# Kernel optimization log

Hardware: AMD Instinct MI355X
Metric: run time of the kernel (lower is better)

The kernel has to match this reference:

```python
import jax, jax.numpy as jnp
import numpy as np

B, S, H, NH, NL = 8, 768, 768, 12, 5
HD = H // NH


def setup_inputs() -> dict:
    key = jax.random.key(0)
    ks = jax.random.split(key, 14)
    lim = 1.0 / np.sqrt(H)
    u = lambda k, shape: jax.random.uniform(k, shape, jnp.float32, -lim, lim)
    inp = {}
    inp["hidden_states"] = jax.random.normal(ks[0], (B, S, H), jnp.float32)
    inp["language_ids"] = jax.random.randint(ks[1], (B,), 0, NL)
    inp["attention_mask"] = jnp.ones((B, S), jnp.int32)
    # per-language query/key Linear weights (torch Linear: y = x @ W.T + b)
    inp["Wq_lang"] = u(ks[2], (NL, H, H))
    inp["bq_lang"] = u(ks[3], (NL, H))
    inp["Wk_lang"] = u(ks[4], (NL, H, H))
    inp["bk_lang"] = u(ks[5], (NL, H))
    # nn.MultiheadAttention params
    inp["in_proj_w"] = u(ks[6], (3 * H, H))
    inp["in_proj_b"] = u(ks[7], (3 * H,))
    inp["out_proj_w"] = u(ks[8], (H, H))
    inp["out_proj_b"] = u(ks[9], (H,))
    # alignment matrices: initialized as eye in torch; perturb so products are non-trivial
    inp["align"] = jnp.eye(H, dtype=jnp.float32) + 0.02 * jax.random.normal(ks[10], (NL, NL, H, H), jnp.float32)
    # output projection + layer norm
    inp["proj_w"] = u(ks[11], (H, H))
    inp["proj_b"] = u(ks[12], (H,))
    inp["ln_g"] = jnp.ones((H,), jnp.float32)
    inp["ln_b"] = jnp.zeros((H,), jnp.float32)
    return inp


def reference(hidden_states, language_ids, attention_mask, Wq_lang, bq_lang, Wk_lang, bk_lang,
              in_proj_w, in_proj_b, out_proj_w, out_proj_b, align, proj_w, proj_b, ln_g, ln_b):
    b, s, h = hidden_states.shape
    lang = language_ids
    # language-routed query/key transforms (grouped GEMM via gather of per-lang weights)
    q = jnp.einsum('bsi,boi->bso', hidden_states, Wq_lang[lang]) + bq_lang[lang][:, None, :]
    k = jnp.einsum('bsi,boi->bso', hidden_states, Wk_lang[lang]) + bk_lang[lang][:, None, :]
    # nn.MultiheadAttention (eval mode, no dropout). Note: the torch module's
    # key_padding_mask is always all-False due to a masked_fill(-inf).bool() bug,
    # so no masking is applied -- reproduced faithfully here.
    wq, wk, wv = jnp.split(in_proj_w, 3, axis=0)
    bq_, bk_, bv_ = jnp.split(in_proj_b, 3)
    Q = (jnp.einsum('bsi,oi->bso', q, wq) + bq_).reshape(b, s, NH, HD)
    K = (jnp.einsum('bsi,oi->bso', k, wk) + bk_).reshape(b, s, NH, HD)
    V = (jnp.einsum('bsi,oi->bso', hidden_states, wv) + bv_).reshape(b, s, NH, HD)
    scores = jnp.einsum('bqhd,bkhd->bhqk', Q, K) / np.sqrt(HD).astype(np.float32)
    attn = jax.nn.softmax(scores, axis=-1)  # [b, nh, s, s]
    ctx = jnp.einsum('bhqk,bkhd->bqhd', attn, V).reshape(b, s, h)
    aligned = jnp.einsum('bsi,oi->bso', ctx, out_proj_w) + out_proj_b
    # pairwise alignment chain: for each i, aligned_i @ prod_{j: lang_j != lang_i} A[lang_i, lang_j]
    # (i==j skipped; same-language pairs skipped since no A exists)
    same = lang[:, None] == lang[None, :]  # [b, b]; diagonal is True -> identity
    sel = align[lang[:, None], lang[None, :]]  # [b, b, h, h]
    I = jnp.eye(h, dtype=hidden_states.dtype)
    Smat = jnp.where(same[:, :, None, None], I, sel)  # [b(i), b(j), h, h]
    def step(carry, Sj):  # carry [b,h,h], Sj [b,h,h] for one j across all i
        return carry @ Sj, None
    M, _ = jax.lax.scan(step, jnp.tile(I, (b, 1, 1)), jnp.swapaxes(Smat, 0, 1))
    aligned = jnp.einsum('bsh,bhk->bsk', aligned, M)
    # output projection + residual layer norm
    out = jnp.einsum('bsi,oi->bso', aligned, proj_w) + proj_b
    x = out + hidden_states
    mu = x.mean(-1, keepdims=True)
    var = x.var(-1, keepdims=True)
    return (x - mu) / jnp.sqrt(var + 1e-5) * ln_g + ln_b
```

## Files before the change

### kernel.cpp

```cpp
#include <hip/hip_runtime.h>

#define Bn 8
#define Sn 768
#define Hn 768
#define NHn 12
#define HDn 64
#define NLn 5

typedef unsigned short u16;
typedef __bf16 bf16x8 __attribute__((ext_vector_type(8)));
typedef short s16x8 __attribute__((ext_vector_type(8)));
typedef float f32x4 __attribute__((ext_vector_type(4)));
typedef unsigned short u16x4 __attribute__((ext_vector_type(4)));

static __device__ __forceinline__ float bf2f(u16 v) {
    return __uint_as_float(((unsigned)v) << 16);
}
static __device__ __forceinline__ u16 f2bf(float f) {
    unsigned u = __float_as_uint(f);
    unsigned r = u + 0x7fffu + ((u >> 16) & 1u);
    return (u16)(r >> 16);
}
static __device__ __forceinline__ bf16x8 ld8(const u16* p) {
    return *reinterpret_cast<const bf16x8*>(p);
}
static __device__ __forceinline__ void glds16(const u16* g, u16* l) {
    __builtin_amdgcn_global_load_lds(
        (const __attribute__((address_space(1))) void*)g,
        (__attribute__((address_space(3))) void*)l, 16, 0, 0);
}

#define PREP_NF2B 6912
#define PREP_NTR  1584
__global__ __launch_bounds__(256) void k_prep(
    const float* __restrict__ hidden, u16* __restrict__ hb,
    const float* __restrict__ ipw, u16* __restrict__ ipwb,
    const float* __restrict__ projw, u16* __restrict__ pjwb,
    const float* __restrict__ Wq, const float* __restrict__ Wk,
    const float* __restrict__ opw, u16* __restrict__ S, u16* __restrict__ opwT,
    const float* __restrict__ ipb,
    const float* __restrict__ bq_lang, const float* __restrict__ bk_lang,
    float* __restrict__ beff)
{
    __shared__ float T[64][65];
    const size_t HH = (size_t)Hn * Hn;
    const int bid = blockIdx.x, tid = threadIdx.x;
    if (bid < PREP_NF2B) {
        const int n0 = (int)(Bn * Sn * Hn / 4), n1 = (int)(3 * HH / 4), n2 = (int)(HH / 4);
        int i = bid * 256 + tid;
        const float* s; u16* d; int off;
        if (i < n0)                { s = hidden; d = hb;   off = i; }
        else if (i < n0 + n1)      { s = ipw;    d = ipwb; off = i - n0; }
        else if (i < n0 + n1 + n2) { s = projw;  d = pjwb; off = i - n0 - n1; }
        else return;
        float4 v = reinterpret_cast<const float4*>(s)[off];
        u16x4 o;
        o[0] = f2bf(v.x); o[1] = f2bf(v.y); o[2] = f2bf(v.z); o[3] = f2bf(v.w);
        reinterpret_cast<u16x4*>(d)[off] = o;
    } else if (bid < PREP_NF2B + PREP_NTR) {
        int b2 = bid - PREP_NF2B;
        int z = b2 / 144, r = b2 % 144;
        int bx = r % 12, by = r / 12;
        const float* src;
        u16* dst;
        if (z < 5)       { src = Wq + (size_t)z * HH;       dst = S + (size_t)z * HH; }
        else if (z < 10) { src = Wk + (size_t)(z - 5) * HH; dst = S + (size_t)z * HH; }
        else             { src = opw;                        dst = opwT; }
        int i0 = bx * 64, o0 = by * 64;
        int x = tid & 63, ys = tid >> 6;
        for (int rr = ys; rr < 64; rr += 4)
            T[rr][x] = src[(size_t)(o0 + rr) * Hn + i0 + x];
        __syncthreads();
        for (int rr = ys; rr < 64; rr += 4)
            dst[(size_t)(i0 + rr) * Hn + o0 + x] = f2bf(T[x][rr]);
    } else {
        int b3 = bid - PREP_NF2B - PREP_NTR;
        int ox = b3 % 3, y = b3 / 3;
        int o = ox * 256 + tid;
        int which = y / 5, l = y % 5;
        const float4* w = reinterpret_cast<const float4*>(ipw + (size_t)which * HH + (size_t)o * Hn);
        const float4* bv = reinterpret_cast<const float4*>(((which ? bk_lang : bq_lang) + (size_t)l * Hn));
        float s = 0.f;
        for (int j = 0; j < Hn / 4; ++j) {
            float4 a = w[j], b = bv[j];
            s += a.x * b.x + a.y * b.y + a.z * b.z + a.w * b.w;
        }
        s += ipb[which * Hn + o];
        beff[(size_t)(which * 5 + l) * Hn + o] = s;
    }
}

template<int TM>
__device__ __forceinline__ void gemm_core(
    const u16* __restrict__ A, int lda,
    const u16* __restrict__ Bw, int ldb,
    const float* __restrict__ bias,
    const float* __restrict__ addres,
    u16* __restrict__ outH, float* __restrict__ outF,
    u16* __restrict__ outVT, int ldc,
    int m0, int n0, float scale)
{
    constexpr int MI = TM / 32;
    constexpr int AIT = TM / 64;
    __shared__ u16 As[3 * TM * 32];
    __shared__ u16 Bs[3 * 128 * 32];
    const int tid = threadIdx.x;
    const int lane = tid & 63, wave = tid >> 6;
    const int lrow = lane & 15, lquad = lane >> 4;
    const int wm = (wave >> 1) * (TM / 2), wn = (wave & 1) * 64;

    const u16* gA = A + (size_t)(m0 + (tid >> 2)) * lda + (tid & 3) * 8;
    const u16* gB = Bw + (size_t)(n0 + (tid >> 2)) * ldb + (tid & 3) * 8;

    f32x4 z = {0.f, 0.f, 0.f, 0.f};
    f32x4 acc[MI][4];
    #pragma unroll
    for (int i = 0; i < MI; ++i)
        #pragma unroll
        for (int j = 0; j < 4; ++j) acc[i][j] = z;

    auto stage = [&](int bs, int k0) {
        #pragma unroll
        for (int it = 0; it < AIT; ++it)
            glds16(gA + (size_t)(it * 64) * lda + k0, &As[bs * TM * 32 + (tid + 256 * it) * 8]);
        #pragma unroll
        for (int it = 0; it < 2; ++it)
            glds16(gB + (size_t)(it * 64) * ldb + k0, &Bs[bs * 128 * 32 + (tid + 256 * it) * 8]);
    };
    auto compute = [&](int bc) {
        const u16* Ab = &As[bc * TM * 32];
        const u16* Bb = &Bs[bc * 128 * 32];
        bf16x8 af[MI], bf_[4];
        #pragma unroll
        for (int i = 0; i < MI; ++i)
            af[i] = ld8(&Ab[(wm + i * 16 + lrow) * 32 + lquad * 8]);
        #pragma unroll
        for (int j = 0; j < 4; ++j)
            bf_[j] = ld8(&Bb[(wn + j * 16 + lrow) * 32 + lquad * 8]);
        #pragma unroll
        for (int i = 0; i < MI; ++i)
            #pragma unroll
            for (int j = 0; j < 4; ++j)
                acc[i][j] = __builtin_amdgcn_mfma_f32_16x16x32_bf16(af[i], bf_[j], acc[i][j], 0, 0, 0);
    };

    stage(0, 0);
    stage(1, 32);
    int bc = 0, bs = 2;
    for (int kt = 0; kt < 24; ++kt) {
        if (kt < 23) {
            if constexpr (TM == 256) {
                asm volatile("s_waitcnt vmcnt(6)" ::: "memory");
            } else {
                asm volatile("s_waitcnt vmcnt(4)" ::: "memory");
            }
        } else {
            asm volatile("s_waitcnt vmcnt(0)" ::: "memory");
        }
        __builtin_amdgcn_s_barrier();
        if (kt < 22) {
            stage(bs, (kt + 2) * 32);
            bs = (bs == 2) ? 0 : bs + 1;
        }
        compute(bc);
        bc = (bc == 2) ? 0 : bc + 1;
    }

    #pragma unroll
    for (int i = 0; i < MI; ++i) {
        #pragma unroll
        for (int j = 0; j < 4; ++j) {
            int col = n0 + wn + j * 16 + lrow;
            float bv = bias ? bias[col] : 0.f;
            if (outVT) {
                int row0 = m0 + wm + i * 16 + lquad * 4;
                int bb = row0 / Sn, s = row0 % Sn;
                int hh = col >> 6, dd = col & 63;
                u16x4 o;
                #pragma unroll
                for (int r = 0; r < 4; ++r) o[r] = f2bf((acc[i][j][r] + bv) * scale);
                *reinterpret_cast<u16x4*>(
                    outVT + (((size_t)bb * NHn + hh) * 64 + dd) * Sn + s) = o;
            } else {
                #pragma unroll
                for (int r = 0; r < 4; ++r) {
                    int row = m0 + wm + i * 16 + lquad * 4 + r;
                    float v = (acc[i][j][r] + bv) * scale;
                    if (addres) v += addres[(size_t)row * ldc + col];
                    if (outF) outF[(size_t)row * ldc + col] = v;
                    else      outH[(size_t)row * ldc + col] = f2bf(v);
                }
            }
        }
    }
}

__device__ __forceinline__ void gemm64(
    const u16* __restrict__ A, const u16* __restrict__ Bw,
    u16* __restrict__ outH, int m0, int n0)
{
    __shared__ u16 As[3 * 64 * 32];
    __shared__ u16 Bs[3 * 64 * 32];
    const int tid = threadIdx.x;
    const int lane = tid & 63, wave = tid >> 6;
    const int lrow = lane & 15, lquad = lane >> 4;
    const int wm = (wave >> 1) * 32, wn = (wave & 1) * 32;

    const u16* gA = A + (size_t)(m0 + (tid >> 2)) * Hn + (tid & 3) * 8;
    const u16* gB = Bw + (size_t)(n0 + (tid >> 2)) * Hn + (tid & 3) * 8;

    f32x4 z = {0.f, 0.f, 0.f, 0.f};
    f32x4 acc[2][2];
    #pragma unroll
    for (int i = 0; i < 2; ++i)
        #pragma unroll
        for (int j = 0; j < 2; ++j) acc[i][j] = z;

    auto stage = [&](int bs, int k0) {
        glds16(gA + k0, &As[bs * 64 * 32 + tid * 8]);
        glds16(gB + k0, &Bs[bs * 64 * 32 + tid * 8]);
    };
    auto compute = [&](int bc) {
        const u16* Ab = &As[bc * 64 * 32];
        const u16* Bb = &Bs[bc * 64 * 32];
        bf16x8 af[2], bf_[2];
        #pragma unroll
        for (int i = 0; i < 2; ++i)
            af[i] = ld8(&Ab[(wm + i * 16 + lrow) * 32 + lquad * 8]);
        #pragma unroll
        for (int j = 0; j < 2; ++j)
            bf_[j] = ld8(&Bb[(wn + j * 16 + lrow) * 32 + lquad * 8]);
        #pragma unroll
        for (int i = 0; i < 2; ++i)
            #pragma unroll
            for (int j = 0; j < 2; ++j)
                acc[i][j] = __builtin_amdgcn_mfma_f32_16x16x32_bf16(af[i], bf_[j], acc[i][j], 0, 0, 0);
    };

    stage(0, 0);
    stage(1, 32);
    int bc = 0, bs = 2;
    for (int kt = 0; kt < 24; ++kt) {
        if (kt < 23) {
            asm volatile("s_waitcnt vmcnt(2)" ::: "memory");
        } else {
            asm volatile("s_waitcnt vmcnt(0)" ::: "memory");
        }
        __builtin_amdgcn_s_barrier();
        if (kt < 22) {
            stage(bs, (kt + 2) * 32);
            bs = (bs == 2) ? 0 : bs + 1;
        }
        compute(bc);
        bc = (bc == 2) ? 0 : bc + 1;
    }

    #pragma unroll
    for (int i = 0; i < 2; ++i)
        #pragma unroll
        for (int j = 0; j < 2; ++j) {
            int col = n0 + wn + j * 16 + lrow;
            #pragma unroll
            for (int r = 0; r < 4; ++r) {
                int row_ = m0 + wm + i * 16 + lquad * 4 + r;
                outH[(size_t)row_ * Hn + col] = f2bf(acc[i][j][r]);
            }
        }
}


__global__ __launch_bounds__(256, 2) void k_gemm_qkv(
    const u16* __restrict__ A,
    const u16* __restrict__ Sq, const u16* __restrict__ Sk,
    const u16* __restrict__ Wv,
    const float* __restrict__ beff, const float* __restrict__ ipb,
    const int* __restrict__ lang,
    u16* __restrict__ outQ, u16* __restrict__ outK, u16* __restrict__ outVT)
{
    const size_t HH = (size_t)Hn * Hn;
    int z = blockIdx.z;
    int m0 = blockIdx.x * 256, n0 = blockIdx.y * 128;
    int l = lang[blockIdx.x / 3];
    if (z == 0) {
        gemm_core<256>(A, Hn, Sq + (size_t)l * HH, Hn, beff + (size_t)l * Hn,
                       nullptr, outQ, nullptr, nullptr, Hn, m0, n0, 0.125f);
    } else if (z == 1) {
        gemm_core<256>(A, Hn, Sk + (size_t)l * HH, Hn, beff + (size_t)(5 + l) * Hn,
                       nullptr, outK, nullptr, nullptr, Hn, m0, n0, 1.f);
    } else {
        gemm_core<256>(A, Hn, Wv, Hn, ipb + 2 * Hn,
                       nullptr, nullptr, nullptr, outVT, Hn, m0, n0, 1.f);
    }
}

__global__ __launch_bounds__(256) void k_comb10(
    const u16* __restrict__ ipwb, u16* __restrict__ S)
{
    const size_t HH = (size_t)Hn * Hn;
    int z = blockIdx.z;
    const u16* Aop = ipwb + (z < 5 ? 0 : HH);
    gemm_core<128>(Aop, Hn, S + (size_t)z * HH, Hn, nullptr, nullptr,
                   S + (size_t)(10 + z) * HH, nullptr, nullptr, Hn,
                   blockIdx.x * 128, blockIdx.y * 128, 1.f);
}

__global__ __launch_bounds__(256) void k_chain_first(
    const u16* __restrict__ alignb, const int* __restrict__ lang,
    u16* __restrict__ out5)
{
    const size_t HH = (size_t)Hn * Hn;
    int l = blockIdx.z, lj = lang[Bn - 1];
    u16* dst = out5 + (size_t)l * HH;
    int i0 = blockIdx.x * 64, o0 = blockIdx.y * 64;
    const int tid = threadIdx.x;
    if (lj == l) {
        #pragma unroll
        for (int it = 0; it < 2; ++it) {
            int s = tid + 256 * it;
            int ri = s >> 3, c8 = s & 7;
            s16x8 v;
            #pragma unroll
            for (int e = 0; e < 8; ++e)
                v[e] = (short)((i0 + ri == o0 + c8 * 8 + e) ? 0x3F80 : 0);
            *reinterpret_cast<s16x8*>(dst + (size_t)(i0 + ri) * Hn + o0 + c8 * 8) = v;
        }
    } else {
        const u16* src = alignb + ((size_t)l * NLn + lj) * HH;
        __shared__ u16 T[64][72];
        #pragma unroll
        for (int it = 0; it < 2; ++it) {
            int s = tid + 256 * it;
            int r = s >> 3, c8 = s & 7;
            s16x8 v = *reinterpret_cast<const s16x8*>(
                src + (size_t)(o0 + r) * Hn + i0 + c8 * 8);
            #pragma unroll
            for (int e = 0; e < 8; ++e) T[c8 * 8 + e][r] = (u16)v[e];
        }
        __syncthreads();
        #pragma unroll
        for (int it = 0; it < 2; ++it) {
            int s = tid + 256 * it;
            int ri = s >> 3, c8 = s & 7;
            s16x8 v = *reinterpret_cast<const s16x8*>(&T[ri][c8 * 8]);
            *reinterpret_cast<s16x8*>(dst + (size_t)(i0 + ri) * Hn + o0 + c8 * 8) = v;
        }
    }
}

__global__ __launch_bounds__(256) void k_chain64(
    const u16* __restrict__ Pin, u16* __restrict__ Pout,
    const u16* __restrict__ alignb, const int* __restrict__ lang, int j)
{
    const size_t HH = (size_t)Hn * Hn;
    int l = blockIdx.z;
    int lj = lang[j];
    const u16* Pl = Pin + (size_t)l * HH;
    u16* Po = Pout + (size_t)l * HH;
    int m0 = blockIdx.x * 64, n0 = blockIdx.y * 64;
    if (lj == l) {
        int tid = threadIdx.x;
        #pragma unroll
        for (int it = 0; it < 2; ++it) {
            int s = tid + 256 * it;
            int row = s >> 3, seg = s & 7;
            *reinterpret_cast<s16x8*>(Po + (size_t)(m0 + row) * Hn + n0 + seg * 8) =
                *reinterpret_cast<const s16x8*>(Pl + (size_t)(m0 + row) * Hn + n0 + seg * 8);
        }
    } else {
        const u16* F = alignb + ((size_t)l * NLn + lj) * HH;
        gemm64(Pl, F, Po, m0, n0);
    }
}

__global__ __launch_bounds__(256) void k_uop(
    const u16* __restrict__ opwT, const u16* __restrict__ MT5,
    const float* __restrict__ opb,
    u16* __restrict__ U5, float* __restrict__ opbeff)
{
    const size_t HH = (size_t)Hn * Hn;
    int bid = blockIdx.x;
    if (bid < 720) {
        int z = bid / 144, r = bid % 144;
        gemm64(opwT, MT5 + (size_t)z * HH, U5 + (size_t)z * HH,
               (r % 12) * 64, (r / 12) * 64);
    } else {
        int b2 = bid - 720;
        int n = (b2 % 3) * 256 + threadIdx.x;
        int l = b2 / 3;
        const u16* mt = MT5 + ((size_t)l * Hn + n) * Hn;
        float s = 0.f;
        for (int k = 0; k < Hn; k += 8) {
            s16x8 v = *reinterpret_cast<const s16x8*>(mt + k);
            #pragma unroll
            for (int j = 0; j < 8; ++j) s += opb[k + j] * bf2f((u16)v[j]);
        }
        opbeff[(size_t)l * Hn + n] = s;
    }
}

__global__ __launch_bounds__(256) void k_wb2(
    const u16* __restrict__ pjwb, const u16* __restrict__ U5,
    const float* __restrict__ opbeff, const float* __restrict__ projw,
    const float* __restrict__ projb,
    u16* __restrict__ W5, float* __restrict__ bias2)
{
    const size_t HH = (size_t)Hn * Hn;
    int bid = blockIdx.x;
    if (bid < 720) {
        int z = bid / 144, r = bid % 144;
        gemm64(pjwb, U5 + (size_t)z * HH, W5 + (size_t)z * HH,
               (r % 12) * 64, (r / 12) * 64);
    } else {
        int b2 = bid - 720;
        int m = (b2 % 3) * 256 + threadIdx.x;
        int l = b2 / 3;
        const float4* w = reinterpret_cast<const float4*>(projw + (size_t)m * Hn);
        const float4* ob = reinterpret_cast<const float4*>(opbeff + (size_t)l * Hn);
        float s = 0.f;
        for (int j = 0; j < Hn / 4; ++j) {
            float4 a = w[j], b = ob[j];
            s += a.x * b.x + a.y * b.y + a.z * b.z + a.w * b.w;
        }
        bias2[(size_t)l * Hn + m] = s + projb[m];
    }
}

__global__ __launch_bounds__(256) void k_xfused(
    const u16* __restrict__ ctx, const u16* __restrict__ W5,
    const float* __restrict__ bias2, const int* __restrict__ lang,
    const float* __restrict__ hidden, float* __restrict__ x)
{
    int l = lang[blockIdx.x / 6];
    gemm_core<128>(ctx, Hn, W5 + (size_t)l * Hn * Hn, Hn, bias2 + (size_t)l * Hn,
                   hidden, nullptr, x, nullptr, Hn,
                   blockIdx.x * 128, blockIdx.y * 128, 1.f);
}

__global__ __launch_bounds__(512) void k_attn_conv(
    const u16* __restrict__ Q, const u16* __restrict__ K,
    const u16* __restrict__ VT, u16* __restrict__ ctx,
    const float* __restrict__ alignf, u16* __restrict__ alignb)
{
    __shared__ u16 Ks[2][64 * 64];
    __shared__ u16 Vs[2][64 * 64];
    __shared__ u16 Pw[8][16 * 72];

    const int bid = blockIdx.x, tid = threadIdx.x;
    if (bid >= 576) {
        int base = (bid - 576) * 4096 + tid;
        #pragma unroll
        for (int it = 0; it < 8; ++it) {
            int i = base + it * 512;
            float4 v = reinterpret_cast<const float4*>(alignf)[i];
            u16x4 o;
            o[0] = f2bf(v.x); o[1] = f2bf(v.y); o[2] = f2bf(v.z); o[3] = f2bf(v.w);
            reinterpret_cast<u16x4*>(alignb)[i] = o;
        }
        return;
    }

    const int q0 = (bid % 6) * 128, h = (bid / 6) % NHn, bz = bid / 72;
    const int wave = tid >> 6, lane = tid & 63;
    const int lrow = lane & 15, lquad = lane >> 4;
    const int sw = lrow & 7;

    const u16* Qp = Q + ((size_t)(bz * Sn + q0 + wave * 16 + lrow)) * Hn + h * HDn;
    const u16* Kb = K + (size_t)bz * Sn * Hn + h * HDn;
    const u16* Vb = VT + ((size_t)(bz * NHn + h) * 64) * Sn;

    bf16x8 qa0 = ld8(Qp + lquad * 8);
    bf16x8 qa1 = ld8(Qp + 32 + lquad * 8);

    f32x4 z4 = {0.f, 0.f, 0.f, 0.f};
    float m_r[4], l_l[4];
    f32x4 oacc[4];
    #pragma unroll
    for (int r = 0; r < 4; ++r) { m_r[r] = -1e30f; l_l[r] = 0.f; }
    #pragma unroll
    for (int jd = 0; jd < 4; ++jd) oacc[jd] = z4;

    const int krow = tid >> 3, kp = (tid & 7) ^ (krow & 7);
    const u16* kg = Kb + (size_t)krow * Hn + kp * 8;
    const u16* vg = Vb + (size_t)krow * Sn + kp * 8;

    auto stage = [&](int bs, int t0) {
        glds16(kg + (size_t)t0 * Hn, &Ks[bs][tid * 8]);
        glds16(vg + t0, &Vs[bs][tid * 8]);
    };

    auto compute = [&](int bc) {
        f32x4 sc[4];
        __builtin_amdgcn_s_setprio(1);
        #pragma unroll
        for (int j = 0; j < 4; ++j) {
            int base = (j * 16 + lrow) * 64 + ((lquad ^ sw) * 8);
            f32x4 s = __builtin_amdgcn_mfma_f32_16x16x32_bf16(qa0, ld8(&Ks[bc][base]), z4, 0, 0, 0);
            sc[j] = __builtin_amdgcn_mfma_f32_16x16x32_bf16(qa1, ld8(&Ks[bc][base ^ 32]), s, 0, 0, 0);
        }
        __builtin_amdgcn_s_setprio(0);
        float tmax[4];
        #pragma unroll
        for (int r = 0; r < 4; ++r)
            tmax[r] = fmaxf(fmaxf(sc[0][r], sc[1][r]), fmaxf(sc[2][r], sc[3][r]));
        #pragma unroll
        for (int off = 1; off < 16; off <<= 1)
            #pragma unroll
            for (int r = 0; r < 4; ++r)
                tmax[r] = fmaxf(tmax[r], __shfl_xor(tmax[r], off));
        bool grow = (tmax[0] > m_r[0] + 8.f) | (tmax[1] > m_r[1] + 8.f) |
                    (tmax[2] > m_r[2] + 8.f) | (tmax[3] > m_r[3] + 8.f);
        if (grow) {
            #pragma unroll
            for (int r = 0; r < 4; ++r) {
                float mn = fmaxf(m_r[r], tmax[r]);
                float a = __expf(m_r[r] - mn);
                m_r[r] = mn;
                l_l[r] *= a;
                #pragma unroll
                for (int jd = 0; jd < 4; ++jd) oacc[jd][r] *= a;
            }
        }
        float ps[4] = {0.f, 0.f, 0.f, 0.f};
        #pragma unroll
        for (int j = 0; j < 4; ++j)
            #pragma unroll
            for (int r = 0; r < 4; ++r) {
                float p = __expf(sc[j][r] - m_r[r]);
                ps[r] += p;
                Pw[wave][(lquad * 4 + r) * 72 + j * 16 + lrow] = f2bf(p);
            }
        #pragma unroll
        for (int r = 0; r < 4; ++r) l_l[r] += ps[r];
        bf16x8 pa0 = ld8(&Pw[wave][lrow * 72 + lquad * 8]);
        bf16x8 pa1 = ld8(&Pw[wave][lrow * 72 + 32 + lquad * 8]);
        __builtin_amdgcn_s_setprio(1);
        #pragma unroll
        for (int jd = 0; jd < 4; ++jd) {
            int vbase = (jd * 16 + lrow) * 64 + ((lquad ^ sw) * 8);
            oacc[jd] = __builtin_amdgcn_mfma_f32_16x16x32_bf16(pa0, ld8(&Vs[bc][vbase]), oacc[jd], 0, 0, 0);
            oacc[jd] = __builtin_amdgcn_mfma_f32_16x16x32_bf16(pa1, ld8(&Vs[bc][vbase ^ 32]), oacc[jd], 0, 0, 0);
        }
        __builtin_amdgcn_s_setprio(0);
    };

    stage(0, 0);
    stage(1, 64);
    for (int kt = 0; kt < 12; ++kt) {
        if (kt < 11) {
            asm volatile("s_waitcnt vmcnt(2)" ::: "memory");
        } else {
            asm volatile("s_waitcnt vmcnt(0)" ::: "memory");
        }
        __builtin_amdgcn_s_barrier();
        compute(kt & 1);
        if (kt < 10) {
            __builtin_amdgcn_s_barrier();
            stage(kt & 1, (kt + 2) * 64);
        }
    }

    #pragma unroll
    for (int off = 1; off < 16; off <<= 1)
        #pragma unroll
        for (int r = 0; r < 4; ++r)
            l_l[r] += __shfl_xor(l_l[r], off);

    float rl[4];
    #pragma unroll
    for (int r = 0; r < 4; ++r) rl[r] = 1.f / l_l[r];
    #pragma unroll
    for (int jd = 0; jd < 4; ++jd)
        #pragma unroll
        for (int r = 0; r < 4; ++r) {
            size_t row = (size_t)bz * Sn + q0 + wave * 16 + lquad * 4 + r;
            ctx[row * Hn + h * HDn + jd * 16 + lrow] = f2bf(oacc[jd][r] * rl[r]);
        }
}

__global__ __launch_bounds__(64) void k_ln(
    float* x, const float* __restrict__ g, const float* __restrict__ beta)
{
    size_t row = blockIdx.x;
    float* xr = x + row * Hn;
    int lane = threadIdx.x;
    float v[12];
    float s = 0.f, ss = 0.f;
    #pragma unroll
    for (int i = 0; i < 12; ++i) {
        v[i] = xr[lane + i * 64];
        s += v[i];
        ss += v[i] * v[i];
    }
    #pragma unroll
    for (int off = 1; off < 64; off <<= 1) {
        s  += __shfl_xor(s, off);
        ss += __shfl_xor(ss, off);
    }
    float mu = s * (1.f / Hn);
    float var = ss * (1.f / Hn) - mu * mu;
    float inv = rsqrtf(var + 1e-5f);
    #pragma unroll
    for (int i = 0; i < 12; ++i) {
        int c = lane + i * 64;
        xr[c] = (v[i] - mu) * inv * g[c] + beta[c];
    }
}

extern "C" void kernel_launch(void* const* d_in, const int* in_sizes, int n_in,
                              void* d_out, int out_size, void* d_ws, size_t ws_size,
                              hipStream_t stream)
{
    (void)in_sizes; (void)n_in; (void)out_size; (void)ws_size;

    const float* hidden  = (const float*)d_in[0];
    const int*   lang    = (const int*)d_in[1];
    const float* Wq_lang = (const float*)d_in[3];
    const float* bq_lang = (const float*)d_in[4];
    const float* Wk_lang = (const float*)d_in[5];
    const float* bk_lang = (const float*)d_in[6];
    const float* ipw     = (const float*)d_in[7];
    const float* ipb     = (const float*)d_in[8];
    const float* opw     = (const float*)d_in[9];
    const float* opb     = (const float*)d_in[10];
    const float* align   = (const float*)d_in[11];
    const float* projw   = (const float*)d_in[12];
    const float* projb   = (const float*)d_in[13];
    const float* ln_g    = (const float*)d_in[14];
    const float* ln_b    = (const float*)d_in[15];
    float* out = (float*)d_out;

    const size_t HH  = (size_t)Hn * Hn;
    const size_t BSH = (size_t)Bn * Sn * Hn;
    const size_t AHH = (size_t)NLn * NLn * HH;

    u16* rA = (u16*)d_ws;
    u16* rB = rA + BSH;
    u16* rC = rB + BSH;
    u16* rD = rC + BSH;
    u16* ipwb = rD + BSH;
    u16* pjwb = ipwb + 3 * HH;
    u16* opwT = pjwb + HH;
    u16* alignb = opwT + HH;
    float* beff   = (float*)(alignb + AHH);
    float* opbeff = beff + 10 * Hn;
    float* bias2  = opbeff + 5 * Hn;

    u16* S = alignb;

    k_prep<<<(unsigned)(PREP_NF2B + PREP_NTR + 30), 256, 0, stream>>>(
        hidden, rA, ipw, ipwb, projw, pjwb,
        Wq_lang, Wk_lang, opw, S, opwT,
        ipb, bq_lang, bk_lang, beff);

    k_comb10<<<dim3(6, 6, 10), 256, 0, stream>>>(ipwb, S);

    k_gemm_qkv<<<dim3(24, 6, 3), 256, 0, stream>>>(
        rA, S + 10 * HH, S + 15 * HH, ipwb + 2 * HH, beff, ipb, lang, rB, rC, rD);

    k_attn_conv<<<1476, 512, 0, stream>>>(rB, rC, rD, rA, align, alignb);

    k_chain_first<<<dim3(12, 12, NLn), 256, 0, stream>>>(alignb, lang, rC);
    u16* Pin = rC;
    u16* Pout = rD;
    for (int j = Bn - 2; j >= 0; --j) {
        k_chain64<<<dim3(12, 12, NLn), 256, 0, stream>>>(Pin, Pout, alignb, lang, j);
        u16* t = Pin; Pin = Pout; Pout = t;
    }

    k_uop<<<735, 256, 0, stream>>>(opwT, Pin, opb, rB, opbeff);
    k_wb2<<<735, 256, 0, stream>>>(pjwb, rB, opbeff, projw, projb, rC, bias2);

    k_xfused<<<dim3(48, 6), 256, 0, stream>>>(rA, rC, bias2, lang, hidden, out);
    k_ln<<<(unsigned)(Bn * Sn), 64, 0, stream>>>(out, ln_g, ln_b);
}
```

Before: 488.9 us.

## Skip identity chain copies via parity-tracked ping-pong and retile GEMMs smaller

The chain kernel no longer copies the whole matrix when the language matches. Each block instead works out the ping-pong buffer parity from how many non-matching steps came before, and k_uop derives the final buffer from that same count. Several GEMMs move to smaller tiles (qkv 128-row tiles, comb10 and xfused on the 64x64 gemm64) so more blocks are launched. gemm64 gains a bias, residual and fp32-output epilogue to support the xfused path. Smaller tiles give less operand reuse per block in exchange for better occupancy across CUs.

After: 483.0 us. Within noise of the previous version (-1.2%).

```diff
diff --git a/kernel.cpp b/kernel.cpp
--- a/kernel.cpp
+++ b/kernel.cpp
@@ -197,7 +197,9 @@
 
 __device__ __forceinline__ void gemm64(
     const u16* __restrict__ A, const u16* __restrict__ Bw,
-    u16* __restrict__ outH, int m0, int n0)
+    const float* __restrict__ bias, const float* __restrict__ addres,
+    u16* __restrict__ outH, float* __restrict__ outF,
+    int m0, int n0)
 {
     __shared__ u16 As[3 * 64 * 32];
     __shared__ u16 Bs[3 * 64 * 32];
@@ -260,16 +262,20 @@
         #pragma unroll
         for (int j = 0; j < 2; ++j) {
             int col = n0 + wn + j * 16 + lrow;
+            float bv = bias ? bias[col] : 0.f;
             #pragma unroll
             for (int r = 0; r < 4; ++r) {
                 int row_ = m0 + wm + i * 16 + lquad * 4 + r;
-                outH[(size_t)row_ * Hn + col] = f2bf(acc[i][j][r]);
+                float v = acc[i][j][r] + bv;
+                if (addres) v += addres[(size_t)row_ * Hn + col];
+                if (outF) outF[(size_t)row_ * Hn + col] = v;
+                else      outH[(size_t)row_ * Hn + col] = f2bf(v);
             }
         }
 }
 
 
-__global__ __launch_bounds__(256, 2) void k_gemm_qkv(
+__global__ __launch_bounds__(256) void k_gemm_qkv(
     const u16* __restrict__ A,
     const u16* __restrict__ Sq, const u16* __restrict__ Sk,
     const u16* __restrict__ Wv,
@@ -279,16 +285,16 @@
 {
     const size_t HH = (size_t)Hn * Hn;
     int z = blockIdx.z;
-    int m0 = blockIdx.x * 256, n0 = blockIdx.y * 128;
-    int l = lang[blockIdx.x / 3];
+    int m0 = blockIdx.x * 128, n0 = blockIdx.y * 128;
+    int l = lang[blockIdx.x / 6];
     if (z == 0) {
-        gemm_core<256>(A, Hn, Sq + (size_t)l * HH, Hn, beff + (size_t)l * Hn,
+        gemm_core<128>(A, Hn, Sq + (size_t)l * HH, Hn, beff + (size_t)l * Hn,
                        nullptr, outQ, nullptr, nullptr, Hn, m0, n0, 0.125f);
     } else if (z == 1) {
-        gemm_core<256>(A, Hn, Sk + (size_t)l * HH, Hn, beff + (size_t)(5 + l) * Hn,
+        gemm_core<128>(A, Hn, Sk + (size_t)l * HH, Hn, beff + (size_t)(5 + l) * Hn,
                        nullptr, outK, nullptr, nullptr, Hn, m0, n0, 1.f);
     } else {
-        gemm_core<256>(A, Hn, Wv, Hn, ipb + 2 * Hn,
+        gemm_core<128>(A, Hn, Wv, Hn, ipb + 2 * Hn,
                        nullptr, nullptr, nullptr, outVT, Hn, m0, n0, 1.f);
     }
 }
@@ -299,9 +305,9 @@
     const size_t HH = (size_t)Hn * Hn;
     int z = blockIdx.z;
     const u16* Aop = ipwb + (z < 5 ? 0 : HH);
-    gemm_core<128>(Aop, Hn, S + (size_t)z * HH, Hn, nullptr, nullptr,
-                   S + (size_t)(10 + z) * HH, nullptr, nullptr, Hn,
-                   blockIdx.x * 128, blockIdx.y * 128, 1.f);
+    gemm64(Aop, S + (size_t)z * HH, nullptr, nullptr,
+           S + (size_t)(10 + z) * HH, nullptr,
+           blockIdx.x * 64, blockIdx.y * 64);
 }
 
 __global__ __launch_bounds__(256) void k_chain_first(
@@ -348,51 +354,47 @@
 }
 
 __global__ __launch_bounds__(256) void k_chain64(
-    const u16* __restrict__ Pin, u16* __restrict__ Pout,
+    u16* __restrict__ rC, u16* __restrict__ rD,
     const u16* __restrict__ alignb, const int* __restrict__ lang, int j)
 {
     const size_t HH = (size_t)Hn * Hn;
     int l = blockIdx.z;
     int lj = lang[j];
-    const u16* Pl = Pin + (size_t)l * HH;
-    u16* Po = Pout + (size_t)l * HH;
-    int m0 = blockIdx.x * 64, n0 = blockIdx.y * 64;
-    if (lj == l) {
-        int tid = threadIdx.x;
-        #pragma unroll
-        for (int it = 0; it < 2; ++it) {
-            int s = tid + 256 * it;
-            int row = s >> 3, seg = s & 7;
-            *reinterpret_cast<s16x8*>(Po + (size_t)(m0 + row) * Hn + n0 + seg * 8) =
-                *reinterpret_cast<const s16x8*>(Pl + (size_t)(m0 + row) * Hn + n0 + seg * 8);
-        }
-    } else {
-        const u16* F = alignb + ((size_t)l * NLn + lj) * HH;
-        gemm64(Pl, F, Po, m0, n0);
-    }
+    if (lj == l) return;
+    int c = 0;
+    for (int jj = j + 1; jj <= 6; ++jj) c += (lang[jj] != l) ? 1 : 0;
+    const u16* in = ((c & 1) ? rD : rC) + (size_t)l * HH;
+    u16* out = ((c & 1) ? rC : rD) + (size_t)l * HH;
+    const u16* F = alignb + ((size_t)l * NLn + lj) * HH;
+    gemm64(in, F, nullptr, nullptr, out, nullptr,
+           blockIdx.x * 64, blockIdx.y * 64);
 }
 
 __global__ __launch_bounds__(256) void k_uop(
-    const u16* __restrict__ opwT, const u16* __restrict__ MT5,
-    const float* __restrict__ opb,
+    const u16* __restrict__ opwT,
+    const u16* __restrict__ rC, const u16* __restrict__ rD,
+    const int* __restrict__ lang, const float* __restrict__ opb,
     u16* __restrict__ U5, float* __restrict__ opbeff)
 {
     const size_t HH = (size_t)Hn * Hn;
     int bid = blockIdx.x;
+    int l = (bid < 720) ? (bid / 144) : ((bid - 720) / 3);
+    int pf = 0;
+    for (int jj = 0; jj <= 6; ++jj) pf += (lang[jj] != l) ? 1 : 0;
+    const u16* MT = ((pf & 1) ? rD : rC) + (size_t)l * HH;
     if (bid < 720) {
-        int z = bid / 144, r = bid % 144;
-        gemm64(opwT, MT5 + (size_t)z * HH, U5 + (size_t)z * HH,
+        int r = bid % 144;
+        gemm64(opwT, MT, nullptr, nullptr, U5 + (size_t)l * HH, nullptr,
                (r % 12) * 64, (r / 12) * 64);
     } else {
         int b2 = bid - 720;
         int n = (b2 % 3) * 256 + threadIdx.x;
-        int l = b2 / 3;
-        const u16* mt = MT5 + ((size_t)l * Hn + n) * Hn;
+        const u16* mt = MT + (size_t)n * Hn;
         float s = 0.f;
         for (int k = 0; k < Hn; k += 8) {
             s16x8 v = *reinterpret_cast<const s16x8*>(mt + k);
             #pragma unroll
-            for (int j = 0; j < 8; ++j) s += opb[k + j] * bf2f((u16)v[j]);
+            for (int jq = 0; jq < 8; ++jq) s += opb[k + jq] * bf2f((u16)v[jq]);
         }
         opbeff[(size_t)l * Hn + n] = s;
     }
@@ -408,7 +410,8 @@
     int bid = blockIdx.x;
     if (bid < 720) {
         int z = bid / 144, r = bid % 144;
-        gemm64(pjwb, U5 + (size_t)z * HH, W5 + (size_t)z * HH,
+        gemm64(pjwb, U5 + (size_t)z * HH, nullptr, nullptr,
+               W5 + (size_t)z * HH, nullptr,
                (r % 12) * 64, (r / 12) * 64);
     } else {
         int b2 = bid - 720;
@@ -417,8 +420,8 @@
         const float4* w = reinterpret_cast<const float4*>(projw + (size_t)m * Hn);
         const float4* ob = reinterpret_cast<const float4*>(opbeff + (size_t)l * Hn);
         float s = 0.f;
-        for (int j = 0; j < Hn / 4; ++j) {
-            float4 a = w[j], b = ob[j];
+        for (int jq = 0; jq < Hn / 4; ++jq) {
+            float4 a = w[jq], b = ob[jq];
             s += a.x * b.x + a.y * b.y + a.z * b.z + a.w * b.w;
         }
         bias2[(size_t)l * Hn + m] = s + projb[m];
@@ -430,10 +433,10 @@
     const float* __restrict__ bias2, const int* __restrict__ lang,
     const float* __restrict__ hidden, float* __restrict__ x)
 {
-    int l = lang[blockIdx.x / 6];
-    gemm_core<128>(ctx, Hn, W5 + (size_t)l * Hn * Hn, Hn, bias2 + (size_t)l * Hn,
-                   hidden, nullptr, x, nullptr, Hn,
-                   blockIdx.x * 128, blockIdx.y * 128, 1.f);
+    int l = lang[blockIdx.x / 12];
+    gemm64(ctx, W5 + (size_t)l * Hn * Hn, bias2 + (size_t)l * Hn,
+           hidden, nullptr, x,
+           blockIdx.x * 64, blockIdx.y * 64);
 }
 
 __global__ __launch_bounds__(512) void k_attn_conv(
@@ -652,24 +655,20 @@
         Wq_lang, Wk_lang, opw, S, opwT,
         ipb, bq_lang, bk_lang, beff);
 
-    k_comb10<<<dim3(6, 6, 10), 256, 0, stream>>>(ipwb, S);
-
-    k_gemm_qkv<<<dim3(24, 6, 3), 256, 0, stream>>>(
+    k_comb10<<<dim3(12, 12, 10), 256, 0, stream>>>(ipwb, S);
+
+    k_gemm_qkv<<<dim3(48, 6, 3), 256, 0, stream>>>(
         rA, S + 10 * HH, S + 15 * HH, ipwb + 2 * HH, beff, ipb, lang, rB, rC, rD);
 
     k_attn_conv<<<1476, 512, 0, stream>>>(rB, rC, rD, rA, align, alignb);
 
     k_chain_first<<<dim3(12, 12, NLn), 256, 0, stream>>>(alignb, lang, rC);
-    u16* Pin = rC;
-    u16* Pout = rD;
-    for (int j = Bn - 2; j >= 0; --j) {
-        k_chain64<<<dim3(12, 12, NLn), 256, 0, stream>>>(Pin, Pout, alignb, lang, j);
-        u16* t = Pin; Pin = Pout; Pout = t;
-    }
-
-    k_uop<<<735, 256, 0, stream>>>(opwT, Pin, opb, rB, opbeff);
+    for (int j = Bn - 2; j >= 0; --j)
+        k_chain64<<<dim3(12, 12, NLn), 256, 0, stream>>>(rC, rD, alignb, lang, j);
+
+    k_uop<<<735, 256, 0, stream>>>(opwT, rC, rD, lang, opb, rB, opbeff);
     k_wb2<<<735, 256, 0, stream>>>(pjwb, rB, opbeff, projw, projb, rC, bias2);
 
-    k_xfused<<<dim3(48, 6), 256, 0, stream>>>(rA, rC, bias2, lang, hidden, out);
+    k_xfused<<<dim3(96, 12), 256, 0, stream>>>(rA, rC, bias2, lang, hidden, out);
     k_ln<<<(unsigned)(Bn * Sn), 64, 0, stream>>>(out, ln_g, ln_b);
 }
```
